# Performance work log

Hardware: AMD Instinct MI355X
Metric: run time of the kernel (lower is better)

## Reference

```python
import jax, jax.numpy as jnp
import numpy as np
from jax import lax

B = 8      # batch size
R = 64     # voxel grid resolution
DN = ('NDHWC', 'DHWIO', 'NDHWC')  # conv dimension numbers


def setup_inputs() -> dict:
    key = jax.random.key(0)
    ks = jax.random.split(key, 8)
    N = 200000
    # coords: (batch, x, y, z). Sparse active voxels.
    b = jax.random.randint(ks[0], (N, 1), 0, B, dtype=jnp.int32)
    xyz = jax.random.randint(ks[1], (N, 3), 0, R, dtype=jnp.int32)
    coords = jnp.concatenate([b, xyz], axis=1)
    feats = jax.random.normal(ks[2], (N, 1), dtype=jnp.float32)
    W1 = jax.random.normal(ks[3], (3, 3, 3, 1, 32), dtype=jnp.float32) * 0.2
    W2 = jax.random.normal(ks[4], (2, 2, 2, 32, 64), dtype=jnp.float32) * 0.1
    W3 = jax.random.normal(ks[5], (2, 2, 2, 64, 128), dtype=jnp.float32) * 0.07
    fc_w = jax.random.normal(ks[6], (128, 256), dtype=jnp.float32) * 0.09
    fc_b = jnp.zeros((256,), dtype=jnp.float32)
    return {"coords": coords, "feats": feats, "W1": W1, "W2": W2,
            "W3": W3, "fc_w": fc_w, "fc_b": fc_b}


def _pool_mask(m):
    # active-site mask after a stride-2 kernel-2 sparse conv: any active input
    # voxel in the 2x2x2 block activates the output site.
    return lax.reduce_window(m, 0.0, lax.max, (1, 2, 2, 2, 1), (1, 2, 2, 2, 1), 'VALID')


def reference(coords, feats, W1, W2, W3, fc_w, fc_b):
    b, x, y, z = coords[:, 0], coords[:, 1], coords[:, 2], coords[:, 3]
    # Densify the sparse tensor (duplicate coords summed for determinism)
    grid = jnp.zeros((B, R, R, R, 1), feats.dtype).at[b, x, y, z].add(feats)
    mask = jnp.zeros((B, R, R, R, 1), feats.dtype).at[b, x, y, z].set(1.0)

    # Conv3d(1,32,k=3,s=1): submanifold -> output coords == input coords (mask)
    h = lax.conv_general_dilated(grid, W1, (1, 1, 1), 'SAME', dimension_numbers=DN)
    h = jax.nn.relu(h) * mask

    # Conv3d(32,64,k=2,s=2): downsample; active iff any active input in block
    h = lax.conv_general_dilated(h, W2, (2, 2, 2), 'VALID', dimension_numbers=DN)
    mask2 = _pool_mask(mask)
    h = jax.nn.relu(h) * mask2

    # Conv3d(64,128,k=2,s=2)
    h = lax.conv_general_dilated(h, W3, (2, 2, 2), 'VALID', dimension_numbers=DN)
    mask3 = _pool_mask(mask2)
    h = jax.nn.relu(h) * mask3

    # GlobalAvgPool over ACTIVE voxels only, per batch
    s = jnp.sum(h, axis=(1, 2, 3))                       # [B,128]
    cnt = jnp.sum(mask3, axis=(1, 2, 3))                 # [B,1]
    pooled = s / jnp.maximum(cnt, 1.0)

    return pooled @ fc_w + fc_b                          # [B,256]
```

## Files before the change

kernel.cpp:

```cpp
#include <hip/hip_runtime.h>
#include <hip/hip_bf16.h>
#include <hip/hip_fp16.h>

typedef __attribute__((ext_vector_type(2))) _Float16 f16x2;
typedef __attribute__((ext_vector_type(8))) _Float16 f16x8;
typedef __attribute__((ext_vector_type(4))) float    f32x4;

#define GRID_ELEMS (8*64*64*64)

__global__ __launch_bounds__(256) void scatter_setup_k(
    const int* __restrict__ coords, const float* __restrict__ feats,
    const float* __restrict__ W1, const float* __restrict__ W2, const float* __restrict__ W3,
    __half2* __restrict__ gpk,
    uint4* __restrict__ W1f, uint4* __restrict__ W2f,
    uint4* __restrict__ W3fA, uint4* __restrict__ W3fB, int N)
{
  const int bi = blockIdx.x;
  if (bi < 44) {
    const int i = bi * 256 + threadIdx.x;
    if (i < 2048) {
      const int wid = i >> 9, ks = (i >> 6) & 7, lane = i & 63;
      const int l15 = lane & 15, l4 = lane >> 4, o = wid * 16 + l15;
      f16x8 v;
      #pragma unroll
      for (int j = 0; j < 8; ++j)
        v[j] = (_Float16)W2[ks * 2048 + (l4 * 8 + j) * 64 + o];
      W2f[i] = __builtin_bit_cast(uint4, v);
    } else if (i < 10240) {
      const int e = i - 2048, ab = e >> 12, r = e & 4095;
      const int wid = r >> 10, ks = (r >> 6) & 15, lane = r & 63;
      const int l15 = lane & 15, l4 = lane >> 4, o = wid * 32 + l15 + ab * 16;
      f16x8 v;
      #pragma unroll
      for (int j = 0; j < 8; ++j)
        v[j] = (_Float16)W3[(ks >> 1) * 8192 + ((ks & 1) * 32 + l4 * 8 + j) * 128 + o];
      (ab ? W3fB : W3fA)[r] = __builtin_bit_cast(uint4, v);
    } else if (i < 10368) {
      const int t = i - 10240;
      const int mt = t >> 6, l = t & 63;
      f16x8 v;
      #pragma unroll
      for (int j = 0; j < 8; ++j) {
        const int k = (l >> 4) * 8 + j;
        v[j] = (k < 27) ? (_Float16)W1[k * 32 + mt * 16 + (l & 15)] : (_Float16)0;
      }
      W1f[t] = __builtin_bit_cast(uint4, v);
    }
    return;
  }
  const int i = (bi - 44) * 256 + threadIdx.x;
  if (i >= N) return;
  const int4 c = reinterpret_cast<const int4*>(coords)[i];
  const int idx = ((c.x * 64 + c.y) * 64 + c.z) * 64 + c.w;
  const __half2 v = __halves2half2(__float2half_rn(feats[i]), __float2half_rn(1.0f));
  unsafeAtomicAdd(&gpk[idx], v);
}

__global__ __launch_bounds__(256, 6) void mega_k(
    const unsigned* __restrict__ gpk,
    const uint4* __restrict__ W1f, const uint4* __restrict__ W2f,
    const uint4* __restrict__ W3fA, const uint4* __restrict__ W3fB,
    float* __restrict__ spart, float* __restrict__ cntB)
{
  __shared__ unsigned short tile[1008];
  __shared__ float    m1v[512];
  __shared__ unsigned short toff[32];
  __shared__ float    m2s[64];
  __shared__ float    m3s[8];
  __shared__ __align__(16) _Float16 h1f[8192];
  _Float16* const h2s = h1f;

  const int tid = threadIdx.x;
  const int bid = blockIdx.x;
  const int b  = bid >> 9;
  const int X2 = (bid >> 6) & 7, Y2 = (bid >> 3) & 7, Z2 = bid & 7;
  const int gb = b << 18;
  const int lane = tid & 63, wid = tid >> 6;
  const int l15 = lane & 15, l4 = lane >> 4;

  {
    const int gx0 = X2 * 8 - 1, gy0 = Y2 * 8 - 1, gz0 = Z2 * 8 - 1;
    for (int e = tid; e < 1000; e += 256) {
      const int x = e / 100, r = e - x * 100, y = r / 10, z = r - y * 10;
      const int gx = gx0 + x, gy = gy0 + y, gz = gz0 + z;
      const bool ok = ((unsigned)gx < 64u) & ((unsigned)gy < 64u) & ((unsigned)gz < 64u);
      const unsigned g = ok ? gpk[gb + (gx << 12) + (gy << 6) + gz] : 0u;
      tile[e] = (unsigned short)(g & 0xffffu);
      const int ix = x - 1, iy = y - 1, iz = z - 1;
      if (((unsigned)ix < 8u) & ((unsigned)iy < 8u) & ((unsigned)iz < 8u))
        m1v[(ix << 6) + (iy << 3) + iz] = (g >> 16) ? 1.f : 0.f;
    }
  }
  if (tid < 32) {
    unsigned short off = 0;
    if (tid < 27) {
      const int tx = tid / 9, rr = tid - tx * 9, ty = rr / 3, tz = rr - ty * 3;
      off = (unsigned short)((tx * 100 + ty * 10 + tz) * 2);
    }
    toff[tid] = off;
  }

  const uint4 w1a = W1f[lane];
  const uint4 w1b = W1f[64 + lane];
  uint4 w2r[8];
  #pragma unroll
  for (int ks = 0; ks < 8; ++ks) w2r[ks] = W2f[(wid * 8 + ks) * 64 + lane];

  __syncthreads();

  if (wid == 0) {
    const int v2 = lane;
    const int base = ((v2 >> 4) << 7) + (((v2 >> 2) & 3) << 4) + ((v2 & 3) << 1);
    float m = m1v[base];
    m = fmaxf(m, m1v[base + 1]);  m = fmaxf(m, m1v[base + 8]);
    m = fmaxf(m, m1v[base + 9]);  m = fmaxf(m, m1v[base + 64]);
    m = fmaxf(m, m1v[base + 65]); m = fmaxf(m, m1v[base + 72]);
    m = fmaxf(m, m1v[base + 73]);
    m2s[v2] = m;
  }

  int t_off[8];
  #pragma unroll
  for (int j = 0; j < 8; ++j) t_off[j] = toff[l4 * 8 + j];

  const char* tilec = reinterpret_cast<const char*>(tile);
  f32x4 acc[4];
  #pragma unroll
  for (int nt = 0; nt < 4; ++nt) acc[nt] = (f32x4){0.f, 0.f, 0.f, 0.f};

  #pragma unroll
  for (int c = 0; c < 2; ++c) {
    #pragma unroll
    for (int gi = 0; gi < 4; ++gi) {
      const int idx = (wid * 4 + gi) * 16 + l15;
      const int x1 = 2 * (idx >> 6) + c, y1 = (idx >> 3) & 7, z1 = idx & 7;
      const int base2 = (x1 * 100 + y1 * 10 + z1) * 2;
      f16x8 bf;
      #pragma unroll
      for (int j = 0; j < 8; ++j)
        bf[j] = *reinterpret_cast<const _Float16*>(tilec + base2 + t_off[j]);
      f32x4 aA = (f32x4){0.f, 0.f, 0.f, 0.f};
      f32x4 aB = (f32x4){0.f, 0.f, 0.f, 0.f};
      aA = __builtin_amdgcn_mfma_f32_16x16x32_f16(__builtin_bit_cast(f16x8, w1a), bf, aA, 0, 0, 0);
      aB = __builtin_amdgcn_mfma_f32_16x16x32_f16(__builtin_bit_cast(f16x8, w1b), bf, aB, 0, 0, 0);

      const int p_l = ((y1 & 1) << 1) | (z1 & 1);
      const int v2  = ((x1 >> 1) << 4) | ((y1 >> 1) << 2) | (z1 >> 1);
      const float mk = m1v[(x1 << 6) + (y1 << 3) + z1];
      f16x2 mk2; mk2.x = (_Float16)mk; mk2.y = (_Float16)mk;
      const _Float16 z0 = (_Float16)0;
      const int fbase = (((v2 >> 4) * 4 + p_l) * 64 + (v2 & 15)) * 8 + (l4 & 1) * 4;
      const int qsel = l4 >> 1;
      uint2 wA, wB;
      {
        f16x2 t0; t0.x = (_Float16)aA[0]; t0.y = (_Float16)aA[1];
        f16x2 t1; t1.x = (_Float16)aA[2]; t1.y = (_Float16)aA[3];
        t0.x = t0.x > z0 ? t0.x : z0; t0.y = t0.y > z0 ? t0.y : z0;
        t1.x = t1.x > z0 ? t1.x : z0; t1.y = t1.y > z0 ? t1.y : z0;
        t0 = t0 * mk2; t1 = t1 * mk2;
        wA.x = __builtin_bit_cast(unsigned, t0); wA.y = __builtin_bit_cast(unsigned, t1);
      }
      {
        f16x2 t0; t0.x = (_Float16)aB[0]; t0.y = (_Float16)aB[1];
        f16x2 t1; t1.x = (_Float16)aB[2]; t1.y = (_Float16)aB[3];
        t0.x = t0.x > z0 ? t0.x : z0; t0.y = t0.y > z0 ? t0.y : z0;
        t1.x = t1.x > z0 ? t1.x : z0; t1.y = t1.y > z0 ? t1.y : z0;
        t0 = t0 * mk2; t1 = t1 * mk2;
        wB.x = __builtin_bit_cast(unsigned, t0); wB.y = __builtin_bit_cast(unsigned, t1);
      }
      *reinterpret_cast<uint2*>(&h1f[fbase + qsel * 128])       = wA;
      *reinterpret_cast<uint2*>(&h1f[fbase + (2 + qsel) * 128]) = wB;
    }
    __syncthreads();

    #pragma unroll
    for (int ks = 0; ks < 4; ++ks) {
      const f16x8 af = __builtin_bit_cast(f16x8, w2r[c * 4 + ks]);
      #pragma unroll
      for (int nt = 0; nt < 4; ++nt) {
        const f16x8 bb = *reinterpret_cast<const f16x8*>(&h1f[((nt * 4 + ks) * 64 + lane) * 8]);
        acc[nt] = __builtin_amdgcn_mfma_f32_16x16x32_f16(af, bb, acc[nt], 0, 0, 0);
      }
    }
    __syncthreads();
  }

  if (tid < 8) {
    const int x3 = tid >> 2, y3 = (tid >> 1) & 1, z3 = tid & 1;
    float m = 0.f;
    #pragma unroll
    for (int p = 0; p < 8; ++p) {
      const int cv = (((2*x3 + (p>>2)) << 4) | ((2*y3 + ((p>>1)&1)) << 2) | (2*z3 + (p&1)));
      m = fmaxf(m, m2s[cv]);
    }
    m3s[tid] = m;
  }

  uint4 wa[4], wb2[4];
  #pragma unroll
  for (int j = 0; j < 4; ++j) {
    wa[j]  = W3fA[(wid * 16 + j) * 64 + lane];
    wb2[j] = W3fB[(wid * 16 + j) * 64 + lane];
  }

  const int o0 = wid * 16 + l4 * 4;
  #pragma unroll
  for (int nt = 0; nt < 4; ++nt) {
    const int v2l = nt * 16 + l15;
    const float m2v = m2s[v2l];
    const float d0 = fmaxf(acc[nt][0], 0.f) * m2v;
    const float d1 = fmaxf(acc[nt][1], 0.f) * m2v;
    const float d2 = fmaxf(acc[nt][2], 0.f) * m2v;
    const float d3 = fmaxf(acc[nt][3], 0.f) * m2v;
    f16x2 p0; p0.x = (_Float16)d0; p0.y = (_Float16)d1;
    f16x2 p1; p1.x = (_Float16)d2; p1.y = (_Float16)d3;
    uint2 u; u.x = __builtin_bit_cast(unsigned, p0); u.y = __builtin_bit_cast(unsigned, p1);
    *reinterpret_cast<uint2*>(&h2s[v2l * 88 + o0]) = u;
  }
  __syncthreads();

  f32x4 c3a = (f32x4){0.f,0.f,0.f,0.f};
  f32x4 c3b = (f32x4){0.f,0.f,0.f,0.f};
  const int v3 = l15 & 7;
  const int x3o = v3 >> 2, y3o = (v3 >> 1) & 1, z3o = v3 & 1;

  #pragma unroll
  for (int kc = 0; kc < 4; ++kc) {
    uint4 na[4], nb[4];
    if (kc < 3) {
      #pragma unroll
      for (int j = 0; j < 4; ++j) {
        na[j] = W3fA[(wid * 16 + (kc + 1) * 4 + j) * 64 + lane];
        nb[j] = W3fB[(wid * 16 + (kc + 1) * 4 + j) * 64 + lane];
      }
    }
    #pragma unroll
    for (int j = 0; j < 4; ++j) {
      const int ks = kc * 4 + j;
      const int p = ks >> 1;
      const int vox = (((2*x3o + (p>>2)) << 4) | ((2*y3o + ((p>>1)&1)) << 2) | (2*z3o + (p&1)));
      const int c0 = (ks & 1) * 32 + l4 * 8;
      const f16x8 bf = *reinterpret_cast<const f16x8*>(&h2s[vox * 88 + c0]);
      c3a = __builtin_amdgcn_mfma_f32_16x16x32_f16(__builtin_bit_cast(f16x8, wa[j]),  bf, c3a, 0, 0, 0);
      c3b = __builtin_amdgcn_mfma_f32_16x16x32_f16(__builtin_bit_cast(f16x8, wb2[j]), bf, c3b, 0, 0, 0);
    }
    if (kc < 3) {
      #pragma unroll
      for (int j = 0; j < 4; ++j) { wa[j] = na[j]; wb2[j] = nb[j]; }
    }
  }

  const float m3v = (l15 < 8) ? m3s[v3] : 0.f;
  float part[2][4];
  #pragma unroll
  for (int j = 0; j < 4; ++j) {
    part[0][j] = fmaxf(c3a[j], 0.f) * m3v;
    part[1][j] = fmaxf(c3b[j], 0.f) * m3v;
  }
  #pragma unroll
  for (int d = 1; d < 16; d <<= 1) {
    #pragma unroll
    for (int mt = 0; mt < 2; ++mt)
      #pragma unroll
      for (int j = 0; j < 4; ++j)
        part[mt][j] += __shfl_xor(part[mt][j], d, 64);
  }
  if (l15 == 0) {
    const int sb = (b * 64 + (bid & 63)) * 128 + wid * 32;
    #pragma unroll
    for (int mt = 0; mt < 2; ++mt)
      #pragma unroll
      for (int j = 0; j < 4; ++j)
        atomicAdd(&spart[sb + mt * 16 + l4 * 4 + j], part[mt][j]);
  }
  if (tid == 0) {
    float t = 0.f;
    #pragma unroll
    for (int i = 0; i < 8; ++i) t += m3s[i];
    atomicAdd(&cntB[b * 64 + (bid & 63)], t);
  }
}

__global__ __launch_bounds__(256) void reduce_fc_k(
    const float* __restrict__ spart, const float* __restrict__ cntB,
    const float* __restrict__ fc_w, const float* __restrict__ fc_b,
    float* __restrict__ out)
{
  __shared__ float s_l[128];
  __shared__ float c_l;
  const int b = blockIdx.x, tid = threadIdx.x;
  if (tid < 128) {
    float a = 0.f;
    #pragma unroll 8
    for (int g = 0; g < 64; ++g) a += spart[(b * 64 + g) * 128 + tid];
    s_l[tid] = a;
  } else if (tid < 192) {
    float a = cntB[b * 64 + (tid - 128)];
    #pragma unroll
    for (int d = 1; d < 64; d <<= 1) a += __shfl_xor(a, d, 64);
    if (tid == 128) c_l = a;
  }
  __syncthreads();
  const float inv = 1.f / fmaxf(c_l, 1.f);
  float o = fc_b[tid];
  #pragma unroll 8
  for (int c = 0; c < 128; ++c) o = fmaf(s_l[c] * inv, fc_w[c * 256 + tid], o);
  out[b * 256 + tid] = o;
}

extern "C" void kernel_launch(void* const* d_in, const int* in_sizes, int n_in,
                              void* d_out, int out_size, void* d_ws, size_t ws_size,
                              hipStream_t stream)
{
  const int*   coords = (const int*)  d_in[0];
  const float* feats  = (const float*)d_in[1];
  const float* W1     = (const float*)d_in[2];
  const float* W2     = (const float*)d_in[3];
  const float* W3     = (const float*)d_in[4];
  const float* fc_w   = (const float*)d_in[5];
  const float* fc_b   = (const float*)d_in[6];
  float* out = (float*)d_out;
  const int N = in_sizes[0] / 4;

  unsigned* gpk   = (unsigned*)d_ws;
  float*    spart = (float*)(gpk + GRID_ELEMS);
  float*    cntB  = spart + 8 * 64 * 128;
  uint4*    W1f   = (uint4*)(cntB + 512);
  uint4*    W2f   = W1f + 128;
  uint4*    W3fA  = W2f + 2048;
  uint4*    W3fB  = W3fA + 4096;

  hipMemsetAsync(gpk, 0, (size_t)GRID_ELEMS * 4 + 65536 * 4 + 512 * 4, stream);

  scatter_setup_k<<<44 + (N + 255) / 256, 256, 0, stream>>>(
      coords, feats, W1, W2, W3, (__half2*)gpk, W1f, W2f, W3fA, W3fB, N);
  mega_k<<<4096, 256, 0, stream>>>(gpk, W1f, W2f, W3fA, W3fB, spart, cntB);
  reduce_fc_k<<<8, 256, 0, stream>>>(spart, cntB, fc_w, fc_b, out);
}
```

Baseline: 74.74 us.

## Double per-block z extent so conv3 MFMA uses all 16 output columns

Each block now covers an 8x8x16 region, giving 2048 blocks instead of 4096. The 3x3x3 halo tile is loaded once and the conv1/conv2 stages run twice over the two z halves. Both conv2 outputs are kept in LDS so the stride-2 conv3 MFMA fills 16 output voxels, where it previously padded 8 of 16 columns with zeros. The cost is more shared memory (about 36 KB), a lower occupancy hint (4 instead of 6) and more serialized work per block.

Measured after the change: 67.45 us. -9.7%, faster.

```diff
diff --git a/kernel.cpp b/kernel.cpp
--- a/kernel.cpp
+++ b/kernel.cpp
@@ -56,46 +56,46 @@
   unsafeAtomicAdd(&gpk[idx], v);
 }
 
-__global__ __launch_bounds__(256, 6) void mega_k(
+__global__ __launch_bounds__(256, 4) void mega_k(
     const unsigned* __restrict__ gpk,
     const uint4* __restrict__ W1f, const uint4* __restrict__ W2f,
     const uint4* __restrict__ W3fA, const uint4* __restrict__ W3fB,
     float* __restrict__ spart, float* __restrict__ cntB)
 {
-  __shared__ unsigned short tile[1008];
-  __shared__ float    m1v[512];
-  __shared__ unsigned short toff[32];
-  __shared__ float    m2s[64];
-  __shared__ float    m3s[8];
-  __shared__ __align__(16) _Float16 h1f[8192];
-  _Float16* const h2s = h1f;
+  __shared__ __align__(16) char smem[35984];
+  _Float16* const h1f  = (_Float16*)(smem + 11264);
+  _Float16* const tile = (_Float16*)(smem + 27648);
+  float*    const m1v  = (float*)(smem + 31248);
+  float*    const m2s  = (float*)(smem + 35344);
+  float*    const m3s  = (float*)(smem + 35856);
+  unsigned short* const toff = (unsigned short*)(smem + 35920);
 
   const int tid = threadIdx.x;
   const int bid = blockIdx.x;
-  const int b  = bid >> 9;
-  const int X2 = (bid >> 6) & 7, Y2 = (bid >> 3) & 7, Z2 = bid & 7;
-  const int gb = b << 18;
+  const int b   = bid >> 8;
+  const int X2  = (bid >> 5) & 7, Y2 = (bid >> 2) & 7, Zp = bid & 3;
+  const int gb  = b << 18;
   const int lane = tid & 63, wid = tid >> 6;
   const int l15 = lane & 15, l4 = lane >> 4;
 
   {
-    const int gx0 = X2 * 8 - 1, gy0 = Y2 * 8 - 1, gz0 = Z2 * 8 - 1;
-    for (int e = tid; e < 1000; e += 256) {
-      const int x = e / 100, r = e - x * 100, y = r / 10, z = r - y * 10;
+    const int gx0 = X2 * 8 - 1, gy0 = Y2 * 8 - 1, gz0 = Zp * 16 - 1;
+    for (int e = tid; e < 1800; e += 256) {
+      const int x = e / 180, r = e - x * 180, y = r / 18, z = r - y * 18;
       const int gx = gx0 + x, gy = gy0 + y, gz = gz0 + z;
       const bool ok = ((unsigned)gx < 64u) & ((unsigned)gy < 64u) & ((unsigned)gz < 64u);
       const unsigned g = ok ? gpk[gb + (gx << 12) + (gy << 6) + gz] : 0u;
-      tile[e] = (unsigned short)(g & 0xffffu);
+      tile[e] = __builtin_bit_cast(_Float16, (unsigned short)(g & 0xffffu));
       const int ix = x - 1, iy = y - 1, iz = z - 1;
-      if (((unsigned)ix < 8u) & ((unsigned)iy < 8u) & ((unsigned)iz < 8u))
-        m1v[(ix << 6) + (iy << 3) + iz] = (g >> 16) ? 1.f : 0.f;
+      if (((unsigned)ix < 8u) & ((unsigned)iy < 8u) & ((unsigned)iz < 16u))
+        m1v[(ix << 7) + (iy << 4) + iz] = (g >> 16) ? 1.f : 0.f;
     }
   }
   if (tid < 32) {
     unsigned short off = 0;
     if (tid < 27) {
       const int tx = tid / 9, rr = tid - tx * 9, ty = rr / 3, tz = rr - ty * 3;
-      off = (unsigned short)((tx * 100 + ty * 10 + tz) * 2);
+      off = (unsigned short)((tx * 180 + ty * 18 + tz) * 2);
     }
     toff[tid] = off;
   }
@@ -108,121 +108,128 @@
 
   __syncthreads();
 
-  if (wid == 0) {
-    const int v2 = lane;
-    const int base = ((v2 >> 4) << 7) + (((v2 >> 2) & 3) << 4) + ((v2 & 3) << 1);
+  if (tid < 128) {
+    const int base = ((tid >> 5) << 8) + (((tid >> 3) & 3) << 5) + ((tid & 7) << 1);
     float m = m1v[base];
-    m = fmaxf(m, m1v[base + 1]);  m = fmaxf(m, m1v[base + 8]);
-    m = fmaxf(m, m1v[base + 9]);  m = fmaxf(m, m1v[base + 64]);
-    m = fmaxf(m, m1v[base + 65]); m = fmaxf(m, m1v[base + 72]);
-    m = fmaxf(m, m1v[base + 73]);
-    m2s[v2] = m;
+    m = fmaxf(m, m1v[base + 1]);   m = fmaxf(m, m1v[base + 16]);
+    m = fmaxf(m, m1v[base + 17]);  m = fmaxf(m, m1v[base + 128]);
+    m = fmaxf(m, m1v[base + 129]); m = fmaxf(m, m1v[base + 144]);
+    m = fmaxf(m, m1v[base + 145]);
+    m2s[tid] = m;
   }
 
   int t_off[8];
   #pragma unroll
   for (int j = 0; j < 8; ++j) t_off[j] = toff[l4 * 8 + j];
 
-  const char* tilec = reinterpret_cast<const char*>(tile);
-  f32x4 acc[4];
-  #pragma unroll
-  for (int nt = 0; nt < 4; ++nt) acc[nt] = (f32x4){0.f, 0.f, 0.f, 0.f};
-
-  #pragma unroll
-  for (int c = 0; c < 2; ++c) {
-    #pragma unroll
-    for (int gi = 0; gi < 4; ++gi) {
-      const int idx = (wid * 4 + gi) * 16 + l15;
-      const int x1 = 2 * (idx >> 6) + c, y1 = (idx >> 3) & 7, z1 = idx & 7;
-      const int base2 = (x1 * 100 + y1 * 10 + z1) * 2;
-      f16x8 bf;
-      #pragma unroll
-      for (int j = 0; j < 8; ++j)
-        bf[j] = *reinterpret_cast<const _Float16*>(tilec + base2 + t_off[j]);
-      f32x4 aA = (f32x4){0.f, 0.f, 0.f, 0.f};
-      f32x4 aB = (f32x4){0.f, 0.f, 0.f, 0.f};
-      aA = __builtin_amdgcn_mfma_f32_16x16x32_f16(__builtin_bit_cast(f16x8, w1a), bf, aA, 0, 0, 0);
-      aB = __builtin_amdgcn_mfma_f32_16x16x32_f16(__builtin_bit_cast(f16x8, w1b), bf, aB, 0, 0, 0);
-
-      const int p_l = ((y1 & 1) << 1) | (z1 & 1);
-      const int v2  = ((x1 >> 1) << 4) | ((y1 >> 1) << 2) | (z1 >> 1);
-      const float mk = m1v[(x1 << 6) + (y1 << 3) + z1];
-      f16x2 mk2; mk2.x = (_Float16)mk; mk2.y = (_Float16)mk;
-      const _Float16 z0 = (_Float16)0;
-      const int fbase = (((v2 >> 4) * 4 + p_l) * 64 + (v2 & 15)) * 8 + (l4 & 1) * 4;
-      const int qsel = l4 >> 1;
-      uint2 wA, wB;
-      {
-        f16x2 t0; t0.x = (_Float16)aA[0]; t0.y = (_Float16)aA[1];
-        f16x2 t1; t1.x = (_Float16)aA[2]; t1.y = (_Float16)aA[3];
-        t0.x = t0.x > z0 ? t0.x : z0; t0.y = t0.y > z0 ? t0.y : z0;
-        t1.x = t1.x > z0 ? t1.x : z0; t1.y = t1.y > z0 ? t1.y : z0;
-        t0 = t0 * mk2; t1 = t1 * mk2;
-        wA.x = __builtin_bit_cast(unsigned, t0); wA.y = __builtin_bit_cast(unsigned, t1);
-      }
-      {
-        f16x2 t0; t0.x = (_Float16)aB[0]; t0.y = (_Float16)aB[1];
-        f16x2 t1; t1.x = (_Float16)aB[2]; t1.y = (_Float16)aB[3];
-        t0.x = t0.x > z0 ? t0.x : z0; t0.y = t0.y > z0 ? t0.y : z0;
-        t1.x = t1.x > z0 ? t1.x : z0; t1.y = t1.y > z0 ? t1.y : z0;
-        t0 = t0 * mk2; t1 = t1 * mk2;
-        wB.x = __builtin_bit_cast(unsigned, t0); wB.y = __builtin_bit_cast(unsigned, t1);
-      }
-      *reinterpret_cast<uint2*>(&h1f[fbase + qsel * 128])       = wA;
-      *reinterpret_cast<uint2*>(&h1f[fbase + (2 + qsel) * 128]) = wB;
-    }
-    __syncthreads();
-
-    #pragma unroll
-    for (int ks = 0; ks < 4; ++ks) {
-      const f16x8 af = __builtin_bit_cast(f16x8, w2r[c * 4 + ks]);
-      #pragma unroll
-      for (int nt = 0; nt < 4; ++nt) {
-        const f16x8 bb = *reinterpret_cast<const f16x8*>(&h1f[((nt * 4 + ks) * 64 + lane) * 8]);
-        acc[nt] = __builtin_amdgcn_mfma_f32_16x16x32_f16(af, bb, acc[nt], 0, 0, 0);
-      }
-    }
-    __syncthreads();
-  }
-
-  if (tid < 8) {
-    const int x3 = tid >> 2, y3 = (tid >> 1) & 1, z3 = tid & 1;
-    float m = 0.f;
-    #pragma unroll
-    for (int p = 0; p < 8; ++p) {
-      const int cv = (((2*x3 + (p>>2)) << 4) | ((2*y3 + ((p>>1)&1)) << 2) | (2*z3 + (p&1)));
-      m = fmaxf(m, m2s[cv]);
-    }
-    m3s[tid] = m;
-  }
-
+  const char* tilec = (const char*)tile;
   uint4 wa[4], wb2[4];
-  #pragma unroll
-  for (int j = 0; j < 4; ++j) {
-    wa[j]  = W3fA[(wid * 16 + j) * 64 + lane];
-    wb2[j] = W3fB[(wid * 16 + j) * 64 + lane];
-  }
-
-  const int o0 = wid * 16 + l4 * 4;
-  #pragma unroll
-  for (int nt = 0; nt < 4; ++nt) {
-    const int v2l = nt * 16 + l15;
-    const float m2v = m2s[v2l];
-    const float d0 = fmaxf(acc[nt][0], 0.f) * m2v;
-    const float d1 = fmaxf(acc[nt][1], 0.f) * m2v;
-    const float d2 = fmaxf(acc[nt][2], 0.f) * m2v;
-    const float d3 = fmaxf(acc[nt][3], 0.f) * m2v;
-    f16x2 p0; p0.x = (_Float16)d0; p0.y = (_Float16)d1;
-    f16x2 p1; p1.x = (_Float16)d2; p1.y = (_Float16)d3;
-    uint2 u; u.x = __builtin_bit_cast(unsigned, p0); u.y = __builtin_bit_cast(unsigned, p1);
-    *reinterpret_cast<uint2*>(&h2s[v2l * 88 + o0]) = u;
+
+  #pragma unroll
+  for (int o = 0; o < 2; ++o) {
+    f32x4 acc[4];
+    #pragma unroll
+    for (int nt = 0; nt < 4; ++nt) acc[nt] = (f32x4){0.f, 0.f, 0.f, 0.f};
+
+    #pragma unroll
+    for (int c = 0; c < 2; ++c) {
+      #pragma unroll
+      for (int gi = 0; gi < 4; ++gi) {
+        const int idx = (wid * 4 + gi) * 16 + l15;
+        const int x1 = 2 * (idx >> 6) + c, y1 = (idx >> 3) & 7, zo = idx & 7;
+        const int z1 = o * 8 + zo;
+        const int base2 = (x1 * 180 + y1 * 18 + z1) * 2;
+        f16x8 bf;
+        #pragma unroll
+        for (int j = 0; j < 8; ++j)
+          bf[j] = *reinterpret_cast<const _Float16*>(tilec + base2 + t_off[j]);
+        f32x4 aA = (f32x4){0.f, 0.f, 0.f, 0.f};
+        f32x4 aB = (f32x4){0.f, 0.f, 0.f, 0.f};
+        aA = __builtin_amdgcn_mfma_f32_16x16x32_f16(__builtin_bit_cast(f16x8, w1a), bf, aA, 0, 0, 0);
+        aB = __builtin_amdgcn_mfma_f32_16x16x32_f16(__builtin_bit_cast(f16x8, w1b), bf, aB, 0, 0, 0);
+
+        const int p_l = ((y1 & 1) << 1) | (zo & 1);
+        const int v2  = ((x1 >> 1) << 4) | ((y1 >> 1) << 2) | (zo >> 1);
+        const float mk = m1v[(x1 << 7) + (y1 << 4) + z1];
+        f16x2 mk2; mk2.x = (_Float16)mk; mk2.y = (_Float16)mk;
+        const _Float16 z0 = (_Float16)0;
+        const int fbase = (((v2 >> 4) * 4 + p_l) * 64 + (v2 & 15)) * 8 + (l4 & 1) * 4;
+        const int qsel = l4 >> 1;
+        uint2 wA, wB;
+        {
+          f16x2 t0; t0.x = (_Float16)aA[0]; t0.y = (_Float16)aA[1];
+          f16x2 t1; t1.x = (_Float16)aA[2]; t1.y = (_Float16)aA[3];
+          t0.x = t0.x > z0 ? t0.x : z0; t0.y = t0.y > z0 ? t0.y : z0;
+          t1.x = t1.x > z0 ? t1.x : z0; t1.y = t1.y > z0 ? t1.y : z0;
+          t0 = t0 * mk2; t1 = t1 * mk2;
+          wA.x = __builtin_bit_cast(unsigned, t0); wA.y = __builtin_bit_cast(unsigned, t1);
+        }
+        {
+          f16x2 t0; t0.x = (_Float16)aB[0]; t0.y = (_Float16)aB[1];
+          f16x2 t1; t1.x = (_Float16)aB[2]; t1.y = (_Float16)aB[3];
+          t0.x = t0.x > z0 ? t0.x : z0; t0.y = t0.y > z0 ? t0.y : z0;
+          t1.x = t1.x > z0 ? t1.x : z0; t1.y = t1.y > z0 ? t1.y : z0;
+          t0 = t0 * mk2; t1 = t1 * mk2;
+          wB.x = __builtin_bit_cast(unsigned, t0); wB.y = __builtin_bit_cast(unsigned, t1);
+        }
+        *reinterpret_cast<uint2*>(&h1f[fbase + qsel * 128])       = wA;
+        *reinterpret_cast<uint2*>(&h1f[fbase + (2 + qsel) * 128]) = wB;
+      }
+      __syncthreads();
+
+      if (o == 0 && c == 0 && tid < 16) {
+        const int base = ((tid >> 3) << 6) + (((tid >> 2) & 1) << 4) + ((tid & 3) << 1);
+        float m = m2s[base];
+        m = fmaxf(m, m2s[base + 1]);  m = fmaxf(m, m2s[base + 8]);
+        m = fmaxf(m, m2s[base + 9]);  m = fmaxf(m, m2s[base + 32]);
+        m = fmaxf(m, m2s[base + 33]); m = fmaxf(m, m2s[base + 40]);
+        m = fmaxf(m, m2s[base + 41]);
+        m3s[tid] = m;
+      }
+
+      #pragma unroll
+      for (int ks = 0; ks < 4; ++ks) {
+        const f16x8 af = __builtin_bit_cast(f16x8, w2r[c * 4 + ks]);
+        #pragma unroll
+        for (int nt = 0; nt < 4; ++nt) {
+          const f16x8 bb = *reinterpret_cast<const f16x8*>(&h1f[((nt * 4 + ks) * 64 + lane) * 8]);
+          acc[nt] = __builtin_amdgcn_mfma_f32_16x16x32_f16(af, bb, acc[nt], 0, 0, 0);
+        }
+      }
+
+      if (o == 1 && c == 1) {
+        #pragma unroll
+        for (int j = 0; j < 4; ++j) {
+          wa[j]  = W3fA[(wid * 16 + j) * 64 + lane];
+          wb2[j] = W3fB[(wid * 16 + j) * 64 + lane];
+        }
+      }
+      __syncthreads();
+    }
+
+    _Float16* const h2o = (_Float16*)(smem + o * 11264);
+    const int o0 = wid * 16 + l4 * 4;
+    #pragma unroll
+    for (int nt = 0; nt < 4; ++nt) {
+      const int v2l = nt * 16 + l15;
+      const float m2v = m2s[((v2l >> 4) << 5) + (((v2l >> 2) & 3) << 3) + o * 4 + (v2l & 3)];
+      const float d0 = fmaxf(acc[nt][0], 0.f) * m2v;
+      const float d1 = fmaxf(acc[nt][1], 0.f) * m2v;
+      const float d2 = fmaxf(acc[nt][2], 0.f) * m2v;
+      const float d3 = fmaxf(acc[nt][3], 0.f) * m2v;
+      f16x2 p0; p0.x = (_Float16)d0; p0.y = (_Float16)d1;
+      f16x2 p1; p1.x = (_Float16)d2; p1.y = (_Float16)d3;
+      uint2 u; u.x = __builtin_bit_cast(unsigned, p0); u.y = __builtin_bit_cast(unsigned, p1);
+      *reinterpret_cast<uint2*>(&h2o[v2l * 88 + o0]) = u;
+    }
   }
   __syncthreads();
 
   f32x4 c3a = (f32x4){0.f,0.f,0.f,0.f};
   f32x4 c3b = (f32x4){0.f,0.f,0.f,0.f};
-  const int v3 = l15 & 7;
-  const int x3o = v3 >> 2, y3o = (v3 >> 1) & 1, z3o = v3 & 1;
+  const int v3 = l15;
+  const int x3 = v3 >> 3, y3 = (v3 >> 2) & 1, z3 = v3 & 3;
+  const int obyte = (z3 >> 1) * 11264;
 
   #pragma unroll
   for (int kc = 0; kc < 4; ++kc) {
@@ -238,9 +245,11 @@
     for (int j = 0; j < 4; ++j) {
       const int ks = kc * 4 + j;
       const int p = ks >> 1;
-      const int vox = (((2*x3o + (p>>2)) << 4) | ((2*y3o + ((p>>1)&1)) << 2) | (2*z3o + (p&1)));
+      const int x2 = 2 * x3 + (p >> 2), y2 = 2 * y3 + ((p >> 1) & 1);
+      const int z2l = 2 * (z3 & 1) + (p & 1);
+      const int v2l = (x2 << 4) | (y2 << 2) | z2l;
       const int c0 = (ks & 1) * 32 + l4 * 8;
-      const f16x8 bf = *reinterpret_cast<const f16x8*>(&h2s[vox * 88 + c0]);
+      const f16x8 bf = *reinterpret_cast<const f16x8*>(smem + obyte + (v2l * 88 + c0) * 2);
       c3a = __builtin_amdgcn_mfma_f32_16x16x32_f16(__builtin_bit_cast(f16x8, wa[j]),  bf, c3a, 0, 0, 0);
       c3b = __builtin_amdgcn_mfma_f32_16x16x32_f16(__builtin_bit_cast(f16x8, wb2[j]), bf, c3b, 0, 0, 0);
     }
@@ -250,7 +259,7 @@
     }
   }
 
-  const float m3v = (l15 < 8) ? m3s[v3] : 0.f;
+  const float m3v = m3s[v3];
   float part[2][4];
   #pragma unroll
   for (int j = 0; j < 4; ++j) {
@@ -276,7 +285,7 @@
   if (tid == 0) {
     float t = 0.f;
     #pragma unroll
-    for (int i = 0; i < 8; ++i) t += m3s[i];
+    for (int i = 0; i < 16; ++i) t += m3s[i];
     atomicAdd(&cntB[b * 64 + (bid & 63)], t);
   }
 }
@@ -334,6 +343,6 @@
 
   scatter_setup_k<<<44 + (N + 255) / 256, 256, 0, stream>>>(
       coords, feats, W1, W2, W3, (__half2*)gpk, W1f, W2f, W3fA, W3fB, N);
-  mega_k<<<4096, 256, 0, stream>>>(gpk, W1f, W2f, W3fA, W3fB, spart, cntB);
+  mega_k<<<2048, 256, 0, stream>>>(gpk, W1f, W2f, W3fA, W3fB, spart, cntB);
   reduce_fc_k<<<8, 256, 0, stream>>>(spart, cntB, fc_w, fc_b, out);
 }
```
